# Performance work log

Hardware: AMD Instinct MI355X
Metric: run time of the kernel (lower is better)

Reference implementation:

```python
import jax, jax.numpy as jnp
import numpy as np

B, S, D, E, H, TOPK = 4, 1024, 512, 8, 1536, 2
NORM_EPS = 1e-5

def _ln(x, w, b, eps=1e-5):
    m = jnp.mean(x, -1, keepdims=True)
    v = jnp.var(x, -1, keepdims=True)  # biased var, as torch LayerNorm
    return (x - m) * jax.lax.rsqrt(v + eps) * w + b

def _modulate(x, shift, scale):
    return x * (1 + scale[:, None, :]) + shift[:, None, :]

def setup_inputs() -> dict:
    key = jax.random.key(0)
    ks = jax.random.split(key, 14)
    s = 0.02
    return dict(
        x=jax.random.normal(ks[0], (B, S, D), jnp.float32),
        c=jax.random.normal(ks[1], (B, D), jnp.float32),
        W_ada=jax.random.normal(ks[2], (D, 6 * D), jnp.float32) * s,
        b_ada=jax.random.normal(ks[3], (6 * D,), jnp.float32) * 0.1,
        Wq=jax.random.normal(ks[4], (D, D), jnp.float32) * s,
        Wk=jax.random.normal(ks[5], (D, D), jnp.float32) * s,
        Wv=jax.random.normal(ks[6], (D, D), jnp.float32) * s,
        Wo=jax.random.normal(ks[7], (D, D), jnp.float32) * s,
        qn_w=jnp.ones((D,), jnp.float32), qn_b=jnp.zeros((D,), jnp.float32),
        kn_w=jnp.ones((D,), jnp.float32), kn_b=jnp.zeros((D,), jnp.float32),
        an_w=jnp.ones((D,), jnp.float32), an_b=jnp.zeros((D,), jnp.float32),
        fn_w=jnp.ones((D,), jnp.float32), fn_b=jnp.zeros((D,), jnp.float32),
        Wr=jax.random.normal(ks[8], (D, E), jnp.float32) * s,
        br=jnp.zeros((E,), jnp.float32),
        W1=jax.random.normal(ks[9], (E, D, H), jnp.float32) * s,
        W2=jax.random.normal(ks[10], (E, H, D), jnp.float32) * s,
        W3=jax.random.normal(ks[11], (E, D, H), jnp.float32) * s,
    )

def reference(x, c, W_ada, b_ada, Wq, Wk, Wv, Wo, qn_w, qn_b, kn_w, kn_b,
              an_w, an_b, fn_w, fn_b, Wr, br, W1, W2, W3):
    # adaLN conditioning: SiLU -> Linear -> 6 chunks
    mods = jax.nn.silu(c) @ W_ada + b_ada          # (B, 6D)
    sh_msa, sc_msa, g_msa, sh_mlp, sc_mlp, g_mlp = jnp.split(mods, 6, axis=1)

    # Attention (source attends over the FEATURE dim: scores are (B, D, D))
    h = _modulate(_ln(x, an_w, an_b, NORM_EPS), sh_msa, sc_msa)
    q = _ln(h @ Wq, qn_w, qn_b)
    k = _ln(h @ Wk, kn_w, kn_b)
    v = h @ Wv
    scores = jnp.einsum('bsd,bse->bde', q, k)      # (B, D, D), no 1/sqrt scale (as source)
    A = jax.nn.softmax(scores, axis=-1)
    attn = jnp.einsum('bde,bse->bsd', A, v) @ Wo   # (B, S, D)
    x = x + g_msa[:, None, :] * attn

    # MoE feed-forward (top-2 routing; output REPLACES x, no residual/gate per source)
    xm = _modulate(_ln(x, fn_w, fn_b, NORM_EPS), sh_mlp, sc_mlp)
    logits = xm @ Wr + br                          # (B, S, E)
    # F.normalize default dim=1 -> L2 normalize over the SEQUENCE axis (faithful)
    nrm = jnp.sqrt(jnp.sum(logits * logits, axis=1, keepdims=True))
    logits = logits / jnp.maximum(nrm, 1e-12)
    probs = jax.nn.softmax(logits, axis=-1)        # (B, S, E)
    vals, idx = jax.lax.top_k(probs, TOPK)

    T = B * S
    xf = xm.reshape(T, D)
    # dense combine weights: zero for unselected experts (same math as gather/scatter-add)
    wden = jnp.zeros((T, E), xf.dtype).at[jnp.arange(T)[:, None], idx.reshape(T, TOPK)].set(vals.reshape(T, TOPK))
    h1 = jnp.einsum('td,edh->teh', xf, W1)
    h3 = jnp.einsum('td,edh->teh', xf, W3)
    y = jnp.einsum('teh,ehd->ted', jnp.sin(h1) * h3, W2)  # sin-gated FFN per expert
    moe = jnp.einsum('ted,te->td', y, wden).reshape(B, S, D)

    avg = probs.mean(axis=0)                       # mean over batch dim only (faithful): (S, E)
    aux = jnp.sum((1.0 / E - avg) ** 2)
    return moe, aux
```

## Files before the change

kernel.cpp:

```cpp
#include <hip/hip_runtime.h>
#include <math.h>

#define NB 4
#define NS 1024
#define ND 512
#define NE 8
#define NH 1536
#define NT 4096
#define D6 3072

typedef _Float16 half_t;
typedef _Float16 f16x8 __attribute__((ext_vector_type(8)));
typedef _Float16 f16x4 __attribute__((ext_vector_type(4)));
typedef float    f32x4 __attribute__((ext_vector_type(4)));

#define LDC 136
#define TM_MAX 71

__device__ __forceinline__ void gld16(const void* g, void* l) {
  __builtin_amdgcn_global_load_lds((const __attribute__((address_space(1))) char*)g,
                                   (__attribute__((address_space(3))) char*)l, 16, 0, 0);
}

__device__ __forceinline__ int resolve_tile(const int* __restrict__ offs, int t,
                                            int& e_out, int& m0_out) {
  int acc = 0, found = 0, ee = 0, mm = 0;
  #pragma unroll
  for (int q = 0; q < NE; ++q) {
    int ne_q = offs[q + 1] - offs[q];
    int te = (ne_q + 127) >> 7;
    if (!found && t < acc + te) { ee = q; mm = (t - acc) << 7; found = 1; }
    acc += te;
  }
  e_out = ee; m0_out = mm;
  return found;
}

__global__ __launch_bounds__(256) void k_ada(const float* __restrict__ c,
    const float* __restrict__ Wada, const float* __restrict__ bada,
    float* __restrict__ mods)
{
  __shared__ float sc[ND];
  __shared__ float part[256];
  int tid = threadIdx.x;
  int blk = blockIdx.x;
  int o0 = blk * 64;
  int b = o0 / D6;
  int j0 = o0 - b * D6;
  for (int d = tid; d < ND; d += 256) {
    float v = c[b * ND + d];
    sc[d] = v / (1.f + expf(-v));
  }
  __syncthreads();
  int j = j0 + (tid & 63);
  int kc = tid >> 6;
  float acc = 0.f;
  #pragma unroll 8
  for (int d = kc * 128; d < kc * 128 + 128; ++d)
    acc += sc[d] * Wada[(size_t)d * D6 + j];
  part[tid] = acc;
  __syncthreads();
  if (tid < 64) {
    float r = part[tid] + part[tid + 64] + part[tid + 128] + part[tid + 192]
            + bada[j0 + tid];
    mods[b * D6 + j0 + tid] = r;
  }
}

__global__ __launch_bounds__(256) void k_lnmod(const float* X, int xstride,
    float* Yf, half_t* Yh, half_t* Yl, int ystride,
    const float* __restrict__ w, const float* __restrict__ b,
    const float* __restrict__ mods, int sh_off, int sc_off,
    const float* __restrict__ Wr, const float* __restrict__ br,
    float* __restrict__ logits)
{
  __shared__ float red[16];
  __shared__ float red2[32];
  int tid = threadIdx.x;
  int row = blockIdx.x;
  int batch = row >> 10;
  const float* xr = X + (size_t)row * xstride;
  float x0 = xr[tid], x1 = xr[tid + 256];
  float s = x0 + x1, q = x0 * x0 + x1 * x1;
  #pragma unroll
  for (int off = 32; off > 0; off >>= 1) { s += __shfl_down(s, off, 64); q += __shfl_down(q, off, 64); }
  if ((tid & 63) == 0) { red[tid >> 6] = s; red[8 + (tid >> 6)] = q; }
  __syncthreads();
  if (tid == 0) {
    float S = red[0] + red[1] + red[2] + red[3];
    float Q = red[8] + red[9] + red[10] + red[11];
    float mean = S * (1.f / (float)ND);
    float var = Q * (1.f / (float)ND) - mean * mean;
    red[0] = mean; red[1] = rsqrtf(var + 1e-5f);
  }
  __syncthreads();
  float mean = red[0], rstd = red[1];
  int d0 = tid, d1 = tid + 256;
  float y0 = (x0 - mean) * rstd * w[d0] + b[d0];
  float y1 = (x1 - mean) * rstd * w[d1] + b[d1];
  if (mods) {
    const float* mb = mods + batch * D6;
    y0 = y0 * (1.f + mb[sc_off + d0]) + mb[sh_off + d0];
    y1 = y1 * (1.f + mb[sc_off + d1]) + mb[sh_off + d1];
  }
  size_t o0 = (size_t)row * ystride + d0, o1 = (size_t)row * ystride + d1;
  if (Yf) { Yf[o0] = y0; Yf[o1] = y1; }
  if (Yh) {
    half_t h0 = (half_t)y0, h1 = (half_t)y1;
    Yh[o0] = h0; Yh[o1] = h1;
    if (Yl) { Yl[o0] = (half_t)(y0 - (float)h0); Yl[o1] = (half_t)(y1 - (float)h1); }
  }
  if (Wr) {
    float p[8];
    float4 wa = *(const float4*)(Wr + d0 * 8);
    float4 wb = *(const float4*)(Wr + d0 * 8 + 4);
    float4 wc = *(const float4*)(Wr + d1 * 8);
    float4 wd = *(const float4*)(Wr + d1 * 8 + 4);
    p[0] = y0 * wa.x + y1 * wc.x; p[1] = y0 * wa.y + y1 * wc.y;
    p[2] = y0 * wa.z + y1 * wc.z; p[3] = y0 * wa.w + y1 * wc.w;
    p[4] = y0 * wb.x + y1 * wd.x; p[5] = y0 * wb.y + y1 * wd.y;
    p[6] = y0 * wb.z + y1 * wd.z; p[7] = y0 * wb.w + y1 * wd.w;
    #pragma unroll
    for (int off = 32; off > 0; off >>= 1)
      #pragma unroll
      for (int e = 0; e < 8; ++e) p[e] += __shfl_down(p[e], off, 64);
    if ((tid & 63) == 0) {
      #pragma unroll
      for (int e = 0; e < 8; ++e) red2[(tid >> 6) * 8 + e] = p[e];
    }
    __syncthreads();
    if (tid < 8)
      logits[(size_t)row * 8 + tid] = red2[tid] + red2[8 + tid] + red2[16 + tid]
                                    + red2[24 + tid] + br[tid];
  }
}

__global__ __launch_bounds__(256) void k_lnqk(float* QKV,
    const float* __restrict__ qw, const float* __restrict__ qb,
    const float* __restrict__ kw, const float* __restrict__ kb)
{
  __shared__ float red[16];
  int tid = threadIdx.x;
  int row = blockIdx.x >> 1;
  int h = blockIdx.x & 1;
  const float* w = h ? kw : qw;
  const float* b = h ? kb : qb;
  float* xr = QKV + (size_t)row * 1536 + h * 512;
  float x0 = xr[tid], x1 = xr[tid + 256];
  float s = x0 + x1, q = x0 * x0 + x1 * x1;
  #pragma unroll
  for (int off = 32; off > 0; off >>= 1) { s += __shfl_down(s, off, 64); q += __shfl_down(q, off, 64); }
  if ((tid & 63) == 0) { red[tid >> 6] = s; red[8 + (tid >> 6)] = q; }
  __syncthreads();
  if (tid == 0) {
    float S = red[0] + red[1] + red[2] + red[3];
    float Q = red[8] + red[9] + red[10] + red[11];
    float mean = S * (1.f / (float)ND);
    float var = Q * (1.f / (float)ND) - mean * mean;
    red[0] = mean; red[1] = rsqrtf(var + 1e-5f);
  }
  __syncthreads();
  float mean = red[0], rstd = red[1];
  xr[tid]       = (x0 - mean) * rstd * w[tid] + b[tid];
  xr[tid + 256] = (x1 - mean) * rstd * w[tid + 256] + b[tid + 256];
}

__global__ __launch_bounds__(256) void k_tsplit2(const float* __restrict__ QKV,
    half_t* __restrict__ H0, half_t* __restrict__ L0)
{
  __shared__ float tile[32][33];
  int z = blockIdx.z;
  half_t* outH = H0 + (size_t)z * 4194304;
  half_t* outL = L0 + (size_t)z * 4194304;
  int col0 = z * 512;
  int s0 = blockIdx.x * 32, c0 = blockIdx.y * 32;
  int tid = threadIdx.x;
  int r = tid >> 5, c = tid & 31;
  #pragma unroll
  for (int p = 0; p < 4; ++p)
    tile[r + p * 8][c] = QKV[(size_t)(s0 + r + p * 8) * 1536 + col0 + c0 + c];
  __syncthreads();
  #pragma unroll
  for (int p = 0; p < 4; ++p) {
    float v = tile[c][r + p * 8];
    half_t h = (half_t)v;
    size_t o = (size_t)(c0 + r + p * 8) * NT + s0 + c;
    outH[o] = h; outL[o] = (half_t)(v - (float)h);
  }
}

__global__ __launch_bounds__(256) void k_wsplit4(const float* __restrict__ Wq,
    const float* __restrict__ Wk, const float* __restrict__ Wv,
    const float* __restrict__ Wo, half_t* __restrict__ outH, half_t* __restrict__ outL)
{
  __shared__ float tile[32][33];
  int z = blockIdx.z;
  const float* W = (z == 0) ? Wq : (z == 1) ? Wk : (z == 2) ? Wv : Wo;
  int rowoff = z * 512;
  int k0 = blockIdx.x * 32, n0 = blockIdx.y * 32;
  int tid = threadIdx.x;
  int r = tid >> 5, c = tid & 31;
  #pragma unroll
  for (int p = 0; p < 4; ++p)
    tile[r + p * 8][c] = W[(size_t)(k0 + r + p * 8) * ND + n0 + c];
  __syncthreads();
  #pragma unroll
  for (int p = 0; p < 4; ++p) {
    float v = tile[c][r + p * 8];
    half_t h = (half_t)v;
    size_t o = (size_t)(rowoff + n0 + r + p * 8) * ND + k0 + c;
    outH[o] = h; outL[o] = (half_t)(v - (float)h);
  }
}

__global__ __launch_bounds__(256) void k_vsplit(const float* __restrict__ QKV,
    half_t* __restrict__ Vh, half_t* __restrict__ Vl)
{
  int i = blockIdx.x * 256 + threadIdx.x;
  int s = i >> 7, c = (i & 127) * 4;
  float4 v = *(const float4*)(QKV + (size_t)s * 1536 + 1024 + c);
  f16x4 h, l;
  h[0] = (half_t)v.x; l[0] = (half_t)(v.x - (float)h[0]);
  h[1] = (half_t)v.y; l[1] = (half_t)(v.y - (float)h[1]);
  h[2] = (half_t)v.z; l[2] = (half_t)(v.z - (float)h[2]);
  h[3] = (half_t)v.w; l[3] = (half_t)(v.w - (float)h[3]);
  *(f16x4*)(Vh + (size_t)s * ND + c) = h;
  *(f16x4*)(Vl + (size_t)s * ND + c) = l;
}

template<int MODE>
__global__ __launch_bounds__(256, 2) void k_gemm_hl(
    const half_t* __restrict__ Ah, const half_t* __restrict__ Al, long long sAz,
    const half_t* __restrict__ Bh, const half_t* __restrict__ Bl, long long sBz,
    int lda, int ldb, int K,
    float* __restrict__ Cf, half_t* __restrict__ Ch, half_t* __restrict__ Cl,
    long long sCz, int ldc,
    const float* __restrict__ xres, const float* __restrict__ mods)
{
  int z = blockIdx.z;
  int m0 = blockIdx.x * 128, n0 = blockIdx.y * 128;
  __shared__ __align__(16) char smem[65536];
  half_t* Sh = (half_t*)smem;
  int tid = threadIdx.x;
  int lane = tid & 63, w = tid >> 6;
  int wm = (w >> 1) * 64, wn = (w & 1) * 64;
  int qd = lane >> 4, md = lane & 15;
  int rA0 = tid >> 2;
  int sw = (((tid & 3) ^ ((tid >> 3) & 3)) << 3);

  const half_t* pAh0 = Ah + z * sAz + (size_t)(m0 + rA0) * lda + sw;
  const half_t* pAh1 = pAh0 + (size_t)64 * lda;
  const half_t* pAl0 = Al + z * sAz + (size_t)(m0 + rA0) * lda + sw;
  const half_t* pAl1 = pAl0 + (size_t)64 * lda;
  const half_t* pBh0 = Bh + z * sBz + (size_t)(n0 + rA0) * ldb + sw;
  const half_t* pBh1 = pBh0 + (size_t)64 * ldb;
  const half_t* pBl0 = Bl + z * sBz + (size_t)(n0 + rA0) * ldb + sw;
  const half_t* pBl1 = pBl0 + (size_t)64 * ldb;

  char* dAh = smem + w * 1024;
  char* dAl = smem + 16384 + w * 1024;
  char* dBh = smem + 32768 + w * 1024;
  char* dBl = smem + 49152 + w * 1024;

  f32x4 acc[4][4];
  #pragma unroll
  for (int i = 0; i < 4; ++i)
    #pragma unroll
    for (int j = 0; j < 4; ++j)
      #pragma unroll
      for (int p = 0; p < 4; ++p) acc[i][j][p] = 0.f;

  int swq  = ((qd ^ ((md >> 1) & 3)) << 3);
  int aoff = (wm + md) * 32 + swq;
  int boff = (wn + md) * 32 + swq;

#define GEMM_STAGE(p, kk) do { int kb_ = (kk); int pb_ = (p) * 8192;         \
    gld16(pAh0 + kb_, dAh + pb_); gld16(pAh1 + kb_, dAh + pb_ + 4096);       \
    gld16(pAl0 + kb_, dAl + pb_); gld16(pAl1 + kb_, dAl + pb_ + 4096);       \
    gld16(pBh0 + kb_, dBh + pb_); gld16(pBh1 + kb_, dBh + pb_ + 4096);       \
    gld16(pBl0 + kb_, dBl + pb_); gld16(pBl1 + kb_, dBl + pb_ + 4096); } while (0)

  int iters = K >> 5;
  GEMM_STAGE(0, 0);
  int cur = 0;
  #pragma unroll 1
  for (int it = 0; it < iters; ++it) {
    if (it + 1 < iters) {
      GEMM_STAGE(cur ^ 1, (it + 1) * 32);
      asm volatile("s_waitcnt vmcnt(8)\ns_barrier" ::: "memory");
    } else {
      asm volatile("s_waitcnt vmcnt(0)\ns_barrier" ::: "memory");
    }
    const half_t* Ash = Sh + cur * 4096;
    const half_t* Asl = Sh + 8192  + cur * 4096;
    const half_t* Bsh = Sh + 16384 + cur * 4096;
    const half_t* Bsl = Sh + 24576 + cur * 4096;
    f16x8 ah[4], al[4], bh[4], bl[4];
    #pragma unroll
    for (int i = 0; i < 4; ++i) {
      ah[i] = *(const f16x8*)(Ash + aoff + i * 512);
      al[i] = *(const f16x8*)(Asl + aoff + i * 512);
    }
    #pragma unroll
    for (int j = 0; j < 4; ++j) {
      bh[j] = *(const f16x8*)(Bsh + boff + j * 512);
      bl[j] = *(const f16x8*)(Bsl + boff + j * 512);
    }
    __builtin_amdgcn_s_setprio(1);
    #pragma unroll
    for (int i = 0; i < 4; ++i)
      #pragma unroll
      for (int j = 0; j < 4; ++j) {
        acc[i][j] = __builtin_amdgcn_mfma_f32_16x16x32_f16(ah[i], bh[j], acc[i][j], 0, 0, 0);
        acc[i][j] = __builtin_amdgcn_mfma_f32_16x16x32_f16(ah[i], bl[j], acc[i][j], 0, 0, 0);
        acc[i][j] = __builtin_amdgcn_mfma_f32_16x16x32_f16(al[i], bh[j], acc[i][j], 0, 0, 0);
      }
    __builtin_amdgcn_s_setprio(0);
    asm volatile("s_barrier" ::: "memory");
    cur ^= 1;
  }
#undef GEMM_STAGE

  if (MODE == 1) {
    half_t* Cs = (half_t*)smem;
    __syncthreads();
    #pragma unroll
    for (int i = 0; i < 4; ++i)
      #pragma unroll
      for (int j = 0; j < 4; ++j)
        #pragma unroll
        for (int p = 0; p < 4; ++p)
          Cs[(wm + 16 * i + qd * 4 + p) * LDC + wn + 16 * j + md] = (half_t)acc[i][j][p];
    __syncthreads();
    #pragma unroll
    for (int it2 = 0; it2 < 8; ++it2) {
      int chunk = it2 * 256 + tid;
      int r = chunk >> 4, c8 = (chunk & 15) * 8;
      *(f16x8*)(Ch + z * sCz + (size_t)(m0 + r) * ldc + n0 + c8) = *(const f16x8*)(Cs + r * LDC + c8);
    }
    __syncthreads();
    #pragma unroll
    for (int i = 0; i < 4; ++i)
      #pragma unroll
      for (int j = 0; j < 4; ++j)
        #pragma unroll
        for (int p = 0; p < 4; ++p) {
          float v = acc[i][j][p];
          half_t h = (half_t)v;
          Cs[(wm + 16 * i + qd * 4 + p) * LDC + wn + 16 * j + md] = (half_t)(v - (float)h);
        }
    __syncthreads();
    #pragma unroll
    for (int it2 = 0; it2 < 8; ++it2) {
      int chunk = it2 * 256 + tid;
      int r = chunk >> 4, c8 = (chunk & 15) * 8;
      *(f16x8*)(Cl + z * sCz + (size_t)(m0 + r) * ldc + n0 + c8) = *(const f16x8*)(Cs + r * LDC + c8);
    }
  } else {
    #pragma unroll
    for (int i = 0; i < 4; ++i)
      #pragma unroll
      for (int p = 0; p < 4; ++p) {
        int r = m0 + wm + 16 * i + qd * 4 + p;
        float* cp = Cf + z * sCz + (size_t)r * ldc + n0 + wn + md;
        if (MODE == 2) {
          int batch = r >> 10;
          const float* mb = mods + batch * D6 + 2 * ND;
          const float* xp = xres + (size_t)r * ldc + n0 + wn + md;
          #pragma unroll
          for (int j = 0; j < 4; ++j) {
            int col = wn + md + 16 * j;
            cp[16 * j] = xp[16 * j] + mb[n0 + col] * acc[i][j][p];
          }
        } else {
          #pragma unroll
          for (int j = 0; j < 4; ++j) cp[16 * j] = acc[i][j][p];
        }
      }
  }
}

__global__ __launch_bounds__(256) void k_softmax512_sum4(const float* __restrict__ SC4,
    half_t* __restrict__ Ph, half_t* __restrict__ Pl)
{
  __shared__ float red[16];
  int tid = threadIdx.x;
  int row = blockIdx.x;
  int b = row >> 9, d = row & 511;
  const float* r0 = SC4 + ((size_t)(b * 4 + 0) << 18) + (size_t)d * ND;
  const float* r1 = SC4 + ((size_t)(b * 4 + 1) << 18) + (size_t)d * ND;
  const float* r2 = SC4 + ((size_t)(b * 4 + 2) << 18) + (size_t)d * ND;
  const float* r3 = SC4 + ((size_t)(b * 4 + 3) << 18) + (size_t)d * ND;
  float x0 = r0[tid] + r1[tid] + r2[tid] + r3[tid];
  float x1 = r0[tid + 256] + r1[tid + 256] + r2[tid + 256] + r3[tid + 256];
  float m = fmaxf(x0, x1);
  #pragma unroll
  for (int off = 32; off > 0; off >>= 1) m = fmaxf(m, __shfl_down(m, off, 64));
  if ((tid & 63) == 0) red[tid >> 6] = m;
  __syncthreads();
  if (tid == 0) red[0] = fmaxf(fmaxf(red[0], red[1]), fmaxf(red[2], red[3]));
  __syncthreads();
  m = red[0];
  float e0 = expf(x0 - m), e1 = expf(x1 - m);
  float s = e0 + e1;
  #pragma unroll
  for (int off = 32; off > 0; off >>= 1) s += __shfl_down(s, off, 64);
  if ((tid & 63) == 0) red[8 + (tid >> 6)] = s;
  __syncthreads();
  if (tid == 0) red[8] = red[8] + red[9] + red[10] + red[11];
  __syncthreads();
  float inv = 1.f / red[8];
  float p0 = e0 * inv, p1 = e1 * inv;
  size_t base = (size_t)row * ND;
  half_t h0 = (half_t)p0, h1 = (half_t)p1;
  Ph[base + tid] = h0;       Pl[base + tid] = (half_t)(p0 - (float)h0);
  Ph[base + tid + 256] = h1; Pl[base + tid + 256] = (half_t)(p1 - (float)h1);
}

__global__ __launch_bounds__(256) void k_colnorm(const float* __restrict__ logits,
    float* __restrict__ nrm)
{
  __shared__ float red[8];
  int tid = threadIdx.x;
  int b = blockIdx.x >> 3, e = blockIdx.x & 7;
  float acc = 0.f;
  for (int s = tid; s < NS; s += 256) {
    float l = logits[((size_t)(b << 10) + s) * NE + e];
    acc += l * l;
  }
  #pragma unroll
  for (int off = 32; off > 0; off >>= 1) acc += __shfl_down(acc, off, 64);
  if ((tid & 63) == 0) red[tid >> 6] = acc;
  __syncthreads();
  if (tid == 0) nrm[b * NE + e] = sqrtf(red[0] + red[1] + red[2] + red[3]);
}

__global__ __launch_bounds__(1024) void k_route(const float* __restrict__ logits,
    const float* __restrict__ nrm, float* __restrict__ probs,
    float* __restrict__ wsel, int* __restrict__ offs_g,
    int* __restrict__ list, int* __restrict__ inv)
{
  __shared__ unsigned char sisel[8192];
  __shared__ int cw[8][16][8];
  __shared__ int soffs[9];
  __shared__ float snrm[32];
  int tid = threadIdx.x;
  int lane = tid & 63, wv = tid >> 6;
  if (tid < 32) snrm[tid] = fmaxf(nrm[tid], 1e-12f);
  __syncthreads();
  #pragma unroll 1
  for (int c = 0; c < 4; ++c) {
    int t = c * 1024 + tid;
    int b = t >> 10;
    float p[8];
    float4 l0 = *(const float4*)(logits + (size_t)t * 8);
    float4 l1 = *(const float4*)(logits + (size_t)t * 8 + 4);
    p[0] = l0.x / snrm[b * 8 + 0]; p[1] = l0.y / snrm[b * 8 + 1];
    p[2] = l0.z / snrm[b * 8 + 2]; p[3] = l0.w / snrm[b * 8 + 3];
    p[4] = l1.x / snrm[b * 8 + 4]; p[5] = l1.y / snrm[b * 8 + 5];
    p[6] = l1.z / snrm[b * 8 + 6]; p[7] = l1.w / snrm[b * 8 + 7];
    float mx = p[0];
    #pragma unroll
    for (int e = 1; e < 8; ++e) mx = fmaxf(mx, p[e]);
    float s = 0.f;
    #pragma unroll
    for (int e = 0; e < 8; ++e) { p[e] = expf(p[e] - mx); s += p[e]; }
    float invs = 1.f / s;
    #pragma unroll
    for (int e = 0; e < 8; ++e) { p[e] *= invs; probs[(size_t)t * 8 + e] = p[e]; }
    int i1 = 0;
    #pragma unroll
    for (int e = 1; e < 8; ++e) if (p[e] > p[i1]) i1 = e;
    int i2 = (i1 == 0) ? 1 : 0;
    #pragma unroll
    for (int e = 0; e < 8; ++e) if (e != i1 && p[e] > p[i2]) i2 = e;
    wsel[t * 2] = p[i1]; wsel[t * 2 + 1] = p[i2];
    sisel[t * 2] = (unsigned char)i1; sisel[t * 2 + 1] = (unsigned char)i2;
  }
  __syncthreads();
  #pragma unroll 1
  for (int c = 0; c < 8; ++c) {
    int em = sisel[c * 1024 + tid];
    #pragma unroll
    for (int e = 0; e < 8; ++e) {
      unsigned long long mask = __ballot(em == e);
      if (lane == 0) cw[c][wv][e] = (int)__popcll(mask);
    }
  }
  __syncthreads();
  if (tid < 8) {
    int e = tid, run = 0;
    for (int c = 0; c < 8; ++c)
      for (int w2 = 0; w2 < 16; ++w2) { int v = cw[c][w2][e]; cw[c][w2][e] = run; run += v; }
    soffs[e] = run;
  }
  __syncthreads();
  if (tid == 0) {
    int a = 0;
    #pragma unroll
    for (int e = 0; e < 8; ++e) { int v = soffs[e]; soffs[e] = a; a += v; }
    soffs[8] = a;
  }
  __syncthreads();
  if (tid < 9) offs_g[tid] = soffs[tid];
  #pragma unroll 1
  for (int c = 0; c < 8; ++c) {
    int idx = c * 1024 + tid;
    int em = sisel[idx];
    int rk = 0;
    #pragma unroll
    for (int e = 0; e < 8; ++e) {
      unsigned long long mask = __ballot(em == e);
      if (em == e) rk = (int)__popcll(mask & ((1ull << lane) - 1ull));
    }
    int slot = soffs[em] + cw[c][wv][em] + rk;
    list[slot] = idx >> 1;
    inv[idx] = slot;
  }
}

__global__ __launch_bounds__(256) void k_aux(const float* __restrict__ probs,
    float* __restrict__ outAux)
{
  __shared__ float red[8];
  int tid = threadIdx.x;
  float acc = 0.f;
  for (int s = tid; s < NS; s += 256) {
    #pragma unroll
    for (int e = 0; e < NE; ++e) {
      float a = probs[(size_t)s * NE + e] + probs[(size_t)(NS + s) * NE + e]
              + probs[(size_t)(2 * NS + s) * NE + e] + probs[(size_t)(3 * NS + s) * NE + e];
      float d = 0.125f - a * 0.25f;
      acc += d * d;
    }
  }
  #pragma unroll
  for (int off = 32; off > 0; off >>= 1) acc += __shfl_down(acc, off, 64);
  if ((tid & 63) == 0) red[tid >> 6] = acc;
  __syncthreads();
  if (tid == 0) *outAux = red[0] + red[1] + red[2] + red[3];
}

__global__ __launch_bounds__(256) void k_tcast13(const float* __restrict__ W1,
    const float* __restrict__ W3, half_t* __restrict__ W1t, half_t* __restrict__ W3t)
{
  __shared__ float tile[32][33];
  int z = blockIdx.z;
  int sel = z >> 3, e = z & 7;
  const float* We = (sel ? W3 : W1) + (size_t)e * ND * NH;
  half_t* Wte = (sel ? W3t : W1t) + (size_t)e * ND * NH;
  int k0 = blockIdx.x * 32, n0 = blockIdx.y * 32;
  int tid = threadIdx.x;
  int r = tid >> 5, c = tid & 31;
  #pragma unroll
  for (int p = 0; p < 4; ++p)
    tile[r + p * 8][c] = We[(size_t)(k0 + r + p * 8) * NH + n0 + c];
  __syncthreads();
  #pragma unroll
  for (int p = 0; p < 4; ++p)
    Wte[(size_t)(n0 + r + p * 8) * ND + k0 + c] = (half_t)tile[c][r + p * 8];
}

__global__ __launch_bounds__(256) void k_tcastW2(const float* __restrict__ W,
    half_t* __restrict__ Wt)
{
  __shared__ float tile[32][33];
  const float* We = W + (size_t)blockIdx.z * NH * ND;
  half_t* Wte = Wt + (size_t)blockIdx.z * NH * ND;
  int k0 = blockIdx.x * 32, n0 = blockIdx.y * 32;
  int tid = threadIdx.x;
  int r = tid >> 5, c = tid & 31;
  #pragma unroll
  for (int p = 0; p < 4; ++p)
    tile[r + p * 8][c] = We[(size_t)(k0 + r + p * 8) * ND + n0 + c];
  __syncthreads();
  #pragma unroll
  for (int p = 0; p < 4; ++p)
    Wte[(size_t)(n0 + r + p * 8) * NH + k0 + c] = (half_t)tile[c][r + p * 8];
}

__global__ __launch_bounds__(256, 3) void k_ffn_fused(const half_t* __restrict__ xmh,
    const half_t* __restrict__ W1t, const half_t* __restrict__ W3t,
    const int* __restrict__ list, const int* __restrict__ offs,
    half_t* __restrict__ gate)
{
  int bx = blockIdx.x;
  int n0 = (bx % 12) * 128;
  int t  = bx / 12;
  int e, m0;
  if (!resolve_tile(offs, t, e, m0)) return;
  int base = offs[e], ne = offs[e + 1] - base;

  __shared__ __align__(16) char smem[49664];
  half_t* Sh = (half_t*)smem;
  int* rowt = (int*)(smem + 49152);
  int tid = threadIdx.x;
  if (tid < 128) {
    int rr = m0 + tid;
    rowt[tid] = (rr < ne) ? list[base + rr] : 0;
  }
  __syncthreads();

  int lane = tid & 63, w = tid >> 6;
  int wm = (w >> 1) * 64, wn = (w & 1) * 64;
  int qd = lane >> 4, md = lane & 15;
  int rA0 = tid >> 2;
  int sw = (((tid & 3) ^ ((tid >> 3) & 3)) << 3);
  int tok0 = rowt[rA0], tok1 = rowt[rA0 + 64];

  const half_t* gA0  = xmh + (size_t)tok0 * ND + sw;
  const half_t* gA1  = xmh + (size_t)tok1 * ND + sw;
  const half_t* gB10 = W1t + ((size_t)e * NH + n0 + rA0) * ND + sw;
  const half_t* gB11 = gB10 + (size_t)64 * ND;
  const half_t* gB30 = W3t + ((size_t)e * NH + n0 + rA0) * ND + sw;
  const half_t* gB31 = gB30 + (size_t)64 * ND;

  char* dA  = smem + w * 1024;
  char* dB1 = smem + 16384 + w * 1024;
  char* dB3 = smem + 32768 + w * 1024;

  f32x4 acc1[4][4], acc3[4][4];
  #pragma unroll
  for (int i = 0; i < 4; ++i)
    #pragma unroll
    for (int j = 0; j < 4; ++j)
      #pragma unroll
      for (int p = 0; p < 4; ++p) { acc1[i][j][p] = 0.f; acc3[i][j][p] = 0.f; }

  int swq  = ((qd ^ ((md >> 1) & 3)) << 3);
  int aoff = (wm + md) * 32 + swq;
  int boff = (wn + md) * 32 + swq;

#define FFN_STAGE(p, kk) do { int kb_ = (kk); int pb_ = (p) * 8192;          \
    gld16(gA0  + kb_, dA  + pb_); gld16(gA1  + kb_, dA  + pb_ + 4096);       \
    gld16(gB10 + kb_, dB1 + pb_); gld16(gB11 + kb_, dB1 + pb_ + 4096);       \
    gld16(gB30 + kb_, dB3 + pb_); gld16(gB31 + kb_, dB3 + pb_ + 4096); } while (0)

  FFN_STAGE(0, 0);
  int cur = 0;
  #pragma unroll 1
  for (int it = 0; it < 16; ++it) {
    if (it + 1 < 16) {
      FFN_STAGE(cur ^ 1, (it + 1) * 32);
      asm volatile("s_waitcnt vmcnt(6)\ns_barrier" ::: "memory");
    } else {
      asm volatile("s_waitcnt vmcnt(0)\ns_barrier" ::: "memory");
    }
    const half_t* As  = Sh + cur * 4096;
    const half_t* B1s = Sh + 8192  + cur * 4096;
    const half_t* B3s = Sh + 16384 + cur * 4096;
    f16x8 a[4];
    #pragma unroll
    for (int i = 0; i < 4; ++i) a[i] = *(const f16x8*)(As + aoff + i * 512);
    __builtin_amdgcn_s_setprio(1);
    #pragma unroll
    for (int j = 0; j < 4; ++j) {
      f16x8 b1 = *(const f16x8*)(B1s + boff + j * 512);
      f16x8 b3 = *(const f16x8*)(B3s + boff + j * 512);
      #pragma unroll
      for (int i = 0; i < 4; ++i) {
        acc1[i][j] = __builtin_amdgcn_mfma_f32_16x16x32_f16(a[i], b1, acc1[i][j], 0, 0, 0);
        acc3[i][j] = __builtin_amdgcn_mfma_f32_16x16x32_f16(a[i], b3, acc3[i][j], 0, 0, 0);
      }
    }
    __builtin_amdgcn_s_setprio(0);
    asm volatile("s_barrier" ::: "memory");
    cur ^= 1;
  }
#undef FFN_STAGE

  half_t* Cs = (half_t*)smem;
  #pragma unroll
  for (int i = 0; i < 4; ++i)
    #pragma unroll
    for (int j = 0; j < 4; ++j)
      #pragma unroll
      for (int p = 0; p < 4; ++p) {
        int rr = wm + 16 * i + qd * 4 + p;
        int cc = wn + 16 * j + md;
        Cs[rr * LDC + cc] = (half_t)(__sinf(acc1[i][j][p]) * acc3[i][j][p]);
      }
  __syncthreads();
  #pragma unroll
  for (int it = 0; it < 8; ++it) {
    int chunk = it * 256 + tid;
    int rr = chunk >> 4, c8 = (chunk & 15) * 8;
    if (m0 + rr < ne) {
      *(f16x8*)(gate + (size_t)(base + m0 + rr) * NH + n0 + c8) = *(const f16x8*)(Cs + rr * LDC + c8);
    }
  }
}

__global__ __launch_bounds__(256, 4) void k_moe2_mfma(const half_t* __restrict__ gate,
    const half_t* __restrict__ W2t, const int* __restrict__ offs,
    float* __restrict__ P)
{
  int bx = blockIdx.x;
  int n0 = (bx & 3) * 128;
  int t = bx >> 2;
  int e, m0;
  if (!resolve_tile(offs, t, e, m0)) return;
  int base = offs[e], ne = offs[e + 1] - base;

  __shared__ __align__(16) char smem[32768];
  half_t* Sh = (half_t*)smem;
  int tid = threadIdx.x;
  int lane = tid & 63, w = tid >> 6;
  int wm = (w >> 1) * 64, wn = (w & 1) * 64;
  int qd = lane >> 4, md = lane & 15;
  int rA0 = tid >> 2;
  int sw = (((tid & 3) ^ ((tid >> 3) & 3)) << 3);

  int ar0 = m0 + rA0;      if (ar0 >= ne) ar0 = ne - 1;
  int ar1 = m0 + rA0 + 64; if (ar1 >= ne) ar1 = ne - 1;
  const half_t* gA0 = gate + (size_t)(base + ar0) * NH + sw;
  const half_t* gA1 = gate + (size_t)(base + ar1) * NH + sw;
  const half_t* gB0 = W2t + ((size_t)e * ND + n0 + rA0) * NH + sw;
  const half_t* gB1 = gB0 + (size_t)64 * NH;

  char* dA = smem + w * 1024;
  char* dB = smem + 16384 + w * 1024;

  f32x4 acc[4][4];
  #pragma unroll
  for (int i = 0; i < 4; ++i)
    #pragma unroll
    for (int j = 0; j < 4; ++j)
      #pragma unroll
      for (int p = 0; p < 4; ++p) acc[i][j][p] = 0.f;

  int swq  = ((qd ^ ((md >> 1) & 3)) << 3);
  int aoff = (wm + md) * 32 + swq;
  int boff = (wn + md) * 32 + swq;

#define MOE2_STAGE(p, kk) do { int kb_ = (kk); int pb_ = (p) * 8192;         \
    gld16(gA0 + kb_, dA + pb_); gld16(gA1 + kb_, dA + pb_ + 4096);           \
    gld16(gB0 + kb_, dB + pb_); gld16(gB1 + kb_, dB + pb_ + 4096); } while (0)

  MOE2_STAGE(0, 0);
  int cur = 0;
  #pragma unroll 1
  for (int it = 0; it < 48; ++it) {
    if (it + 1 < 48) {
      MOE2_STAGE(cur ^ 1, (it + 1) * 32);
      asm volatile("s_waitcnt vmcnt(4)\ns_barrier" ::: "memory");
    } else {
      asm volatile("s_waitcnt vmcnt(0)\ns_barrier" ::: "memory");
    }
    const half_t* As = Sh + cur * 4096;
    const half_t* Bs = Sh + 8192 + cur * 4096;
    f16x8 a[4];
    #pragma unroll
    for (int i = 0; i < 4; ++i) a[i] = *(const f16x8*)(As + aoff + i * 512);
    __builtin_amdgcn_s_setprio(1);
    #pragma unroll
    for (int j = 0; j < 4; ++j) {
      f16x8 b = *(const f16x8*)(Bs + boff + j * 512);
      #pragma unroll
      for (int i = 0; i < 4; ++i)
        acc[i][j] = __builtin_amdgcn_mfma_f32_16x16x32_f16(a[i], b, acc[i][j], 0, 0, 0);
    }
    __builtin_amdgcn_s_setprio(0);
    asm volatile("s_barrier" ::: "memory");
    cur ^= 1;
  }
#undef MOE2_STAGE

  #pragma unroll
  for (int i = 0; i < 4; ++i)
    #pragma unroll
    for (int p = 0; p < 4; ++p) {
      int gr = m0 + wm + 16 * i + qd * 4 + p;
      if (gr < ne) {
        float* pp = P + (size_t)(base + gr) * ND + n0 + wn + md;
        #pragma unroll
        for (int j = 0; j < 4; ++j)
          pp[16 * j] = acc[i][j][p];
      }
    }
}

__global__ __launch_bounds__(256) void k_moe_reduce(const float* __restrict__ P,
    const int* __restrict__ inv, const float* __restrict__ wsel,
    float* __restrict__ out)
{
  int i = blockIdx.x * 256 + threadIdx.x;
  int t = i >> 7, d4 = i & 127;
  int s1 = inv[t * 2], s2 = inv[t * 2 + 1];
  float w1 = wsel[t * 2], w2 = wsel[t * 2 + 1];
  const float4* P4 = (const float4*)P;
  float4 a = P4[(size_t)s1 * 128 + d4];
  float4 b = P4[(size_t)s2 * 128 + d4];
  float4 o;
  o.x = w1 * a.x + w2 * b.x;
  o.y = w1 * a.y + w2 * b.y;
  o.z = w1 * a.z + w2 * b.z;
  o.w = w1 * a.w + w2 * b.w;
  ((float4*)out)[i] = o;
}

static const size_t BO_MODS  = 0;
static const size_t BO_HH    = 65536;
static const size_t BO_HL2   = 4259840;
static const size_t BO_PH    = 4259840;
static const size_t BO_PL    = 6357056;
static const size_t BO_WALLH = 8454144;
static const size_t BO_WALLL = 10551296;
static const size_t BO_QKV   = 12648448;
static const size_t BO_A0H   = 12648448;
static const size_t BO_A0L   = 16842752;
static const size_t BO_SC4   = 21037056;
static const size_t BO_X2    = 21037056;
static const size_t BO_XM    = 29425664;
static const size_t BO_QTH   = 37814272;
static const size_t BO_QTL   = 42008576;
static const size_t BO_KTH   = 46202880;
static const size_t BO_KTL   = 50397184;
static const size_t BO_VH    = 54591488;
static const size_t BO_VL    = 58785792;
static const size_t BO_W1T   = 37814272;
static const size_t BO_XMH   = 50397184;
static const size_t BO_W3T   = 65536;
static const size_t BO_GATE  = 12648448;
static const size_t BO_W2T   = 65536;
static const size_t BO_P     = 37814272;
static const size_t BO_LOGI  = 62980096;
static const size_t BO_NRM   = 63111168;
static const size_t BO_PROB  = 63111296;
static const size_t BO_WSEL  = 63242368;
static const size_t BO_INTS  = 63307904;

extern "C" void kernel_launch(void* const* d_in, const int* in_sizes, int n_in,
                              void* d_out, int out_size, void* d_ws, size_t ws_size,
                              hipStream_t stream)
{
  const float* x    = (const float*)d_in[0];
  const float* c    = (const float*)d_in[1];
  const float* Wada = (const float*)d_in[2];
  const float* bada = (const float*)d_in[3];
  const float* Wq   = (const float*)d_in[4];
  const float* Wk   = (const float*)d_in[5];
  const float* Wv   = (const float*)d_in[6];
  const float* Wo   = (const float*)d_in[7];
  const float* qn_w = (const float*)d_in[8];
  const float* qn_b = (const float*)d_in[9];
  const float* kn_w = (const float*)d_in[10];
  const float* kn_b = (const float*)d_in[11];
  const float* an_w = (const float*)d_in[12];
  const float* an_b = (const float*)d_in[13];
  const float* fn_w = (const float*)d_in[14];
  const float* fn_b = (const float*)d_in[15];
  const float* Wr   = (const float*)d_in[16];
  const float* br   = (const float*)d_in[17];
  const float* W1   = (const float*)d_in[18];
  const float* W2   = (const float*)d_in[19];
  const float* W3   = (const float*)d_in[20];
  float* out = (float*)d_out;
  char*  ws8 = (char*)d_ws;
  float* MODS = (float*)(ws8 + BO_MODS);
  half_t* Hh = (half_t*)(ws8 + BO_HH),   *Hl = (half_t*)(ws8 + BO_HL2);
  half_t* Ph = (half_t*)(ws8 + BO_PH),   *Pl = (half_t*)(ws8 + BO_PL);
  half_t* WALLH = (half_t*)(ws8 + BO_WALLH), *WALLL = (half_t*)(ws8 + BO_WALLL);
  half_t* WoTh = WALLH + (size_t)1536 * ND,  *WoTl = WALLL + (size_t)1536 * ND;
  float* QKV = (float*)(ws8 + BO_QKV);
  half_t* A0h = (half_t*)(ws8 + BO_A0H), *A0l = (half_t*)(ws8 + BO_A0L);
  float* SC4 = (float*)(ws8 + BO_SC4);
  float* X2  = (float*)(ws8 + BO_X2);
  float* XM  = (float*)(ws8 + BO_XM);
  half_t* qTh = (half_t*)(ws8 + BO_QTH), *qTl = (half_t*)(ws8 + BO_QTL);
  half_t* kTh = (half_t*)(ws8 + BO_KTH), *kTl = (half_t*)(ws8 + BO_KTL);
  half_t* Vh  = (half_t*)(ws8 + BO_VH),  *Vl  = (half_t*)(ws8 + BO_VL);
  half_t* W1T = (half_t*)(ws8 + BO_W1T);
  half_t* W3T = (half_t*)(ws8 + BO_W3T);
  half_t* W2T = (half_t*)(ws8 + BO_W2T);
  half_t* XMH = (half_t*)(ws8 + BO_XMH);
  half_t* GATEH = (half_t*)(ws8 + BO_GATE);
  float* PBUF = (float*)(ws8 + BO_P);
  float* LOGI = (float*)(ws8 + BO_LOGI);
  float* NRM  = (float*)(ws8 + BO_NRM);
  float* PROB = (float*)(ws8 + BO_PROB);
  float* WSEL = (float*)(ws8 + BO_WSEL);
  int* ib   = (int*)(ws8 + BO_INTS);
  int* offs = ib + 8208;
  int* list = ib + 8224;
  int* inv  = ib + 16416;

  k_ada<<<192, 256, 0, stream>>>(c, Wada, bada, MODS);
  k_wsplit4<<<dim3(16, 16, 4), 256, 0, stream>>>(Wq, Wk, Wv, Wo, WALLH, WALLL);
  k_lnmod<<<NT, 256, 0, stream>>>(x, ND, nullptr, Hh, Hl, ND, an_w, an_b, MODS, 0, 512,
                                  nullptr, nullptr, nullptr);
  k_gemm_hl<0><<<dim3(32, 12, 1), 256, 0, stream>>>(Hh, Hl, 0, WALLH, WALLL, 0,
      ND, ND, ND, QKV, nullptr, nullptr, 0, 1536, nullptr, nullptr);
  k_lnqk<<<2 * NT, 256, 0, stream>>>(QKV, qn_w, qn_b, kn_w, kn_b);
  k_tsplit2<<<dim3(128, 16, 2), 256, 0, stream>>>(QKV, qTh, qTl);
  k_vsplit<<<2048, 256, 0, stream>>>(QKV, Vh, Vl);
  k_gemm_hl<0><<<dim3(4, 4, 16), 256, 0, stream>>>(qTh, qTl, 256, kTh, kTl, 256,
      NT, NT, 256, SC4, nullptr, nullptr, 262144, ND, nullptr, nullptr);
  k_softmax512_sum4<<<2048, 256, 0, stream>>>(SC4, Ph, Pl);
  k_gemm_hl<1><<<dim3(8, 4, 4), 256, 0, stream>>>(Vh, Vl, 524288, Ph, Pl, 262144,
      ND, ND, ND, nullptr, A0h, A0l, 524288, ND, nullptr, nullptr);
  k_gemm_hl<2><<<dim3(32, 4, 1), 256, 0, stream>>>(A0h, A0l, 0, WoTh, WoTl, 0,
      ND, ND, ND, X2, nullptr, nullptr, 0, ND, x, MODS);
  k_lnmod<<<NT, 256, 0, stream>>>(X2, ND, XM, XMH, nullptr, ND, fn_w, fn_b, MODS, 1536, 2048,
                                  Wr, br, LOGI);
  k_colnorm<<<32, 256, 0, stream>>>(LOGI, NRM);
  k_route<<<1, 1024, 0, stream>>>(LOGI, NRM, PROB, WSEL, offs, list, inv);
  k_aux<<<1, 256, 0, stream>>>(PROB, out + (size_t)NT * ND);
  k_tcast13<<<dim3(16, 48, 16), 256, 0, stream>>>(W1, W3, W1T, W3T);
  k_ffn_fused<<<TM_MAX * 12, 256, 0, stream>>>(XMH, W1T, W3T, list, offs, GATEH);
  k_tcastW2<<<dim3(48, 16, 8), 256, 0, stream>>>(W2, W2T);
  k_moe2_mfma<<<TM_MAX * 4, 256, 0, stream>>>(GATEH, W2T, offs, PBUF);
  k_moe_reduce<<<2048, 256, 0, stream>>>(PBUF, inv, WSEL, out);
}
```

Baseline: 394.8 us.

## Halve MoE GEMM N-tiles and load FFN A operand directly into registers

The fused W1/W3 FFN kernel and the W2 expert GEMM drop from 128-wide to 64-wide N tiles, which doubles the grid and cuts LDS use and accumulator registers, so more blocks can be resident per CU. In the FFN kernel the gathered token rows (A operand) are no longer staged through LDS. Each lane loads its MFMA fragment straight from global memory into registers, double-buffered across an unrolled two-stage loop. The cost is that A and B data are each fetched twice as often overall, and the direct gathered loads may be less coalesced.

Measured after the change: 431.7 us. 9.4% more time.

```diff
diff --git a/kernel.cpp b/kernel.cpp
--- a/kernel.cpp
+++ b/kernel.cpp
@@ -15,6 +15,7 @@
 typedef float    f32x4 __attribute__((ext_vector_type(4)));
 
 #define LDC 136
+#define LDC2 72
 #define TM_MAX 71
 
 __device__ __forceinline__ void gld16(const void* g, void* l) {
@@ -585,15 +586,15 @@
     half_t* __restrict__ gate)
 {
   int bx = blockIdx.x;
-  int n0 = (bx % 12) * 128;
-  int t  = bx / 12;
+  int n0 = (bx % 24) * 64;
+  int t  = bx / 24;
   int e, m0;
   if (!resolve_tile(offs, t, e, m0)) return;
   int base = offs[e], ne = offs[e + 1] - base;
 
-  __shared__ __align__(16) char smem[49664];
+  __shared__ __align__(16) char smem[18944];
   half_t* Sh = (half_t*)smem;
-  int* rowt = (int*)(smem + 49152);
+  int* rowt = (int*)(smem + 18432);
   int tid = threadIdx.x;
   if (tid < 128) {
     int rr = m0 + tid;
@@ -602,91 +603,103 @@
   __syncthreads();
 
   int lane = tid & 63, w = tid >> 6;
-  int wm = (w >> 1) * 64, wn = (w & 1) * 64;
+  int wm = (w >> 1) * 64, wn = (w & 1) * 32;
   int qd = lane >> 4, md = lane & 15;
-  int rA0 = tid >> 2;
-  int sw = (((tid & 3) ^ ((tid >> 3) & 3)) << 3);
-  int tok0 = rowt[rA0], tok1 = rowt[rA0 + 64];
-
-  const half_t* gA0  = xmh + (size_t)tok0 * ND + sw;
-  const half_t* gA1  = xmh + (size_t)tok1 * ND + sw;
-  const half_t* gB10 = W1t + ((size_t)e * NH + n0 + rA0) * ND + sw;
-  const half_t* gB11 = gB10 + (size_t)64 * ND;
-  const half_t* gB30 = W3t + ((size_t)e * NH + n0 + rA0) * ND + sw;
-  const half_t* gB31 = gB30 + (size_t)64 * ND;
-
-  char* dA  = smem + w * 1024;
-  char* dB1 = smem + 16384 + w * 1024;
-  char* dB3 = smem + 32768 + w * 1024;
-
-  f32x4 acc1[4][4], acc3[4][4];
+  int rB = tid >> 2;
+  int swB = (((tid & 3) ^ ((rB >> 1) & 3)) << 3);
+
+  const half_t* gB1 = W1t + ((size_t)e * NH + n0 + rB) * ND + swB;
+  const half_t* gB3 = W3t + ((size_t)e * NH + n0 + rB) * ND + swB;
+  char* dB1 = smem + w * 1024;
+  char* dB3 = smem + 8192 + w * 1024;
+
+  const half_t* pa0 = xmh + (size_t)rowt[wm + md] * ND + qd * 8;
+  const half_t* pa1 = xmh + (size_t)rowt[wm + 16 + md] * ND + qd * 8;
+  const half_t* pa2 = xmh + (size_t)rowt[wm + 32 + md] * ND + qd * 8;
+  const half_t* pa3 = xmh + (size_t)rowt[wm + 48 + md] * ND + qd * 8;
+
+  f32x4 acc1[4][2], acc3[4][2];
   #pragma unroll
   for (int i = 0; i < 4; ++i)
     #pragma unroll
-    for (int j = 0; j < 4; ++j)
+    for (int j = 0; j < 2; ++j)
       #pragma unroll
       for (int p = 0; p < 4; ++p) { acc1[i][j][p] = 0.f; acc3[i][j][p] = 0.f; }
 
   int swq  = ((qd ^ ((md >> 1) & 3)) << 3);
-  int aoff = (wm + md) * 32 + swq;
   int boff = (wn + md) * 32 + swq;
 
-#define FFN_STAGE(p, kk) do { int kb_ = (kk); int pb_ = (p) * 8192;          \
-    gld16(gA0  + kb_, dA  + pb_); gld16(gA1  + kb_, dA  + pb_ + 4096);       \
-    gld16(gB10 + kb_, dB1 + pb_); gld16(gB11 + kb_, dB1 + pb_ + 4096);       \
-    gld16(gB30 + kb_, dB3 + pb_); gld16(gB31 + kb_, dB3 + pb_ + 4096); } while (0)
-
-  FFN_STAGE(0, 0);
-  int cur = 0;
+#define FFN_STAGE_B(p, kk) do { int kb_ = (kk);                              \
+    gld16(gB1 + kb_, dB1 + (p) * 4096); gld16(gB3 + kb_, dB3 + (p) * 4096); } while (0)
+#define FFN_LOAD_A(ar, kk) do { int ka_ = (kk);                              \
+    ar[0] = *(const f16x8*)(pa0 + ka_); ar[1] = *(const f16x8*)(pa1 + ka_);  \
+    ar[2] = *(const f16x8*)(pa2 + ka_); ar[3] = *(const f16x8*)(pa3 + ka_); } while (0)
+#define FFN_COMPUTE(cur, ar) do {                                            \
+    const half_t* B1s = Sh + (cur) * 2048;                                   \
+    const half_t* B3s = Sh + 4096 + (cur) * 2048;                            \
+    f16x8 b1[2], b3[2];                                                      \
+    _Pragma("unroll")                                                        \
+    for (int j = 0; j < 2; ++j) {                                            \
+      b1[j] = *(const f16x8*)(B1s + boff + j * 512);                         \
+      b3[j] = *(const f16x8*)(B3s + boff + j * 512);                         \
+    }                                                                        \
+    __builtin_amdgcn_s_setprio(1);                                           \
+    _Pragma("unroll")                                                        \
+    for (int j = 0; j < 2; ++j)                                              \
+      _Pragma("unroll")                                                      \
+      for (int i = 0; i < 4; ++i) {                                          \
+        acc1[i][j] = __builtin_amdgcn_mfma_f32_16x16x32_f16(ar[i], b1[j], acc1[i][j], 0, 0, 0); \
+        acc3[i][j] = __builtin_amdgcn_mfma_f32_16x16x32_f16(ar[i], b3[j], acc3[i][j], 0, 0, 0); \
+      }                                                                      \
+    __builtin_amdgcn_s_setprio(0);                                           \
+  } while (0)
+
+  f16x8 a0_[4], a1_[4];
+  FFN_STAGE_B(0, 0);
+  FFN_LOAD_A(a0_, 0);
   #pragma unroll 1
-  for (int it = 0; it < 16; ++it) {
+  for (int it = 0; it < 16; it += 2) {
     if (it + 1 < 16) {
-      FFN_STAGE(cur ^ 1, (it + 1) * 32);
+      FFN_STAGE_B(1, (it + 1) * 32);
+      FFN_LOAD_A(a1_, (it + 1) * 32);
       asm volatile("s_waitcnt vmcnt(6)\ns_barrier" ::: "memory");
     } else {
       asm volatile("s_waitcnt vmcnt(0)\ns_barrier" ::: "memory");
     }
-    const half_t* As  = Sh + cur * 4096;
-    const half_t* B1s = Sh + 8192  + cur * 4096;
-    const half_t* B3s = Sh + 16384 + cur * 4096;
-    f16x8 a[4];
-    #pragma unroll
-    for (int i = 0; i < 4; ++i) a[i] = *(const f16x8*)(As + aoff + i * 512);
-    __builtin_amdgcn_s_setprio(1);
-    #pragma unroll
-    for (int j = 0; j < 4; ++j) {
-      f16x8 b1 = *(const f16x8*)(B1s + boff + j * 512);
-      f16x8 b3 = *(const f16x8*)(B3s + boff + j * 512);
-      #pragma unroll
-      for (int i = 0; i < 4; ++i) {
-        acc1[i][j] = __builtin_amdgcn_mfma_f32_16x16x32_f16(a[i], b1, acc1[i][j], 0, 0, 0);
-        acc3[i][j] = __builtin_amdgcn_mfma_f32_16x16x32_f16(a[i], b3, acc3[i][j], 0, 0, 0);
-      }
-    }
-    __builtin_amdgcn_s_setprio(0);
+    FFN_COMPUTE(0, a0_);
     asm volatile("s_barrier" ::: "memory");
-    cur ^= 1;
-  }
-#undef FFN_STAGE
+    if (it + 2 < 16) {
+      FFN_STAGE_B(0, (it + 2) * 32);
+      FFN_LOAD_A(a0_, (it + 2) * 32);
+      asm volatile("s_waitcnt vmcnt(6)\ns_barrier" ::: "memory");
+    } else {
+      asm volatile("s_waitcnt vmcnt(0)\ns_barrier" ::: "memory");
+    }
+    FFN_COMPUTE(1, a1_);
+    asm volatile("s_barrier" ::: "memory");
+  }
+#undef FFN_STAGE_B
+#undef FFN_LOAD_A
+#undef FFN_COMPUTE
 
   half_t* Cs = (half_t*)smem;
   #pragma unroll
   for (int i = 0; i < 4; ++i)
     #pragma unroll
-    for (int j = 0; j < 4; ++j)
+    for (int j = 0; j < 2; ++j)
       #pragma unroll
       for (int p = 0; p < 4; ++p) {
         int rr = wm + 16 * i + qd * 4 + p;
         int cc = wn + 16 * j + md;
-        Cs[rr * LDC + cc] = (half_t)(__sinf(acc1[i][j][p]) * acc3[i][j][p]);
+        Cs[rr * LDC2 + cc] = (half_t)(__sinf(acc1[i][j][p]) * acc3[i][j][p]);
       }
   __syncthreads();
   #pragma unroll
-  for (int it = 0; it < 8; ++it) {
+  for (int it = 0; it < 4; ++it) {
     int chunk = it * 256 + tid;
-    int rr = chunk >> 4, c8 = (chunk & 15) * 8;
+    int rr = chunk >> 3, c8 = (chunk & 7) * 8;
     if (m0 + rr < ne) {
-      *(f16x8*)(gate + (size_t)(base + m0 + rr) * NH + n0 + c8) = *(const f16x8*)(Cs + rr * LDC + c8);
+      *(f16x8*)(gate + (size_t)(base + m0 + rr) * NH + n0 + c8) = *(const f16x8*)(Cs + rr * LDC2 + c8);
     }
   }
 }
@@ -696,17 +709,17 @@
     float* __restrict__ P)
 {
   int bx = blockIdx.x;
-  int n0 = (bx & 3) * 128;
-  int t = bx >> 2;
+  int n0 = (bx & 7) * 64;
+  int t = bx >> 3;
   int e, m0;
   if (!resolve_tile(offs, t, e, m0)) return;
   int base = offs[e], ne = offs[e + 1] - base;
 
-  __shared__ __align__(16) char smem[32768];
+  __shared__ __align__(16) char smem[24576];
   half_t* Sh = (half_t*)smem;
   int tid = threadIdx.x;
   int lane = tid & 63, w = tid >> 6;
-  int wm = (w >> 1) * 64, wn = (w & 1) * 64;
+  int wm = (w >> 1) * 64, wn = (w & 1) * 32;
   int qd = lane >> 4, md = lane & 15;
   int rA0 = tid >> 2;
   int sw = (((tid & 3) ^ ((tid >> 3) & 3)) << 3);
@@ -716,16 +729,15 @@
   const half_t* gA0 = gate + (size_t)(base + ar0) * NH + sw;
   const half_t* gA1 = gate + (size_t)(base + ar1) * NH + sw;
   const half_t* gB0 = W2t + ((size_t)e * ND + n0 + rA0) * NH + sw;
-  const half_t* gB1 = gB0 + (size_t)64 * NH;
 
   char* dA = smem + w * 1024;
   char* dB = smem + 16384 + w * 1024;
 
-  f32x4 acc[4][4];
+  f32x4 acc[4][2];
   #pragma unroll
   for (int i = 0; i < 4; ++i)
     #pragma unroll
-    for (int j = 0; j < 4; ++j)
+    for (int j = 0; j < 2; ++j)
       #pragma unroll
       for (int p = 0; p < 4; ++p) acc[i][j][p] = 0.f;
 
@@ -733,9 +745,9 @@
   int aoff = (wm + md) * 32 + swq;
   int boff = (wn + md) * 32 + swq;
 
-#define MOE2_STAGE(p, kk) do { int kb_ = (kk); int pb_ = (p) * 8192;         \
-    gld16(gA0 + kb_, dA + pb_); gld16(gA1 + kb_, dA + pb_ + 4096);           \
-    gld16(gB0 + kb_, dB + pb_); gld16(gB1 + kb_, dB + pb_ + 4096); } while (0)
+#define MOE2_STAGE(p, kk) do { int kb_ = (kk);                               \
+    gld16(gA0 + kb_, dA + (p) * 8192); gld16(gA1 + kb_, dA + (p) * 8192 + 4096); \
+    gld16(gB0 + kb_, dB + (p) * 4096); } while (0)
 
   MOE2_STAGE(0, 0);
   int cur = 0;
@@ -743,23 +755,23 @@
   for (int it = 0; it < 48; ++it) {
     if (it + 1 < 48) {
       MOE2_STAGE(cur ^ 1, (it + 1) * 32);
-      asm volatile("s_waitcnt vmcnt(4)\ns_barrier" ::: "memory");
+      asm volatile("s_waitcnt vmcnt(3)\ns_barrier" ::: "memory");
     } else {
       asm volatile("s_waitcnt vmcnt(0)\ns_barrier" ::: "memory");
     }
     const half_t* As = Sh + cur * 4096;
-    const half_t* Bs = Sh + 8192 + cur * 4096;
-    f16x8 a[4];
+    const half_t* Bs = Sh + 8192 + cur * 2048;
+    f16x8 a[4], b[2];
     #pragma unroll
     for (int i = 0; i < 4; ++i) a[i] = *(const f16x8*)(As + aoff + i * 512);
+    #pragma unroll
+    for (int j = 0; j < 2; ++j) b[j] = *(const f16x8*)(Bs + boff + j * 512);
     __builtin_amdgcn_s_setprio(1);
     #pragma unroll
-    for (int j = 0; j < 4; ++j) {
-      f16x8 b = *(const f16x8*)(Bs + boff + j * 512);
+    for (int j = 0; j < 2; ++j)
       #pragma unroll
       for (int i = 0; i < 4; ++i)
-        acc[i][j] = __builtin_amdgcn_mfma_f32_16x16x32_f16(a[i], b, acc[i][j], 0, 0, 0);
-    }
+        acc[i][j] = __builtin_amdgcn_mfma_f32_16x16x32_f16(a[i], b[j], acc[i][j], 0, 0, 0);
     __builtin_amdgcn_s_setprio(0);
     asm volatile("s_barrier" ::: "memory");
     cur ^= 1;
@@ -774,7 +786,7 @@
       if (gr < ne) {
         float* pp = P + (size_t)(base + gr) * ND + n0 + wn + md;
         #pragma unroll
-        for (int j = 0; j < 4; ++j)
+        for (int j = 0; j < 2; ++j)
           pp[16 * j] = acc[i][j][p];
       }
     }
@@ -907,8 +919,8 @@
   k_route<<<1, 1024, 0, stream>>>(LOGI, NRM, PROB, WSEL, offs, list, inv);
   k_aux<<<1, 256, 0, stream>>>(PROB, out + (size_t)NT * ND);
   k_tcast13<<<dim3(16, 48, 16), 256, 0, stream>>>(W1, W3, W1T, W3T);
-  k_ffn_fused<<<TM_MAX * 12, 256, 0, stream>>>(XMH, W1T, W3T, list, offs, GATEH);
+  k_ffn_fused<<<TM_MAX * 24, 256, 0, stream>>>(XMH, W1T, W3T, list, offs, GATEH);
   k_tcastW2<<<dim3(48, 16, 8), 256, 0, stream>>>(W2, W2T);
-  k_moe2_mfma<<<TM_MAX * 4, 256, 0, stream>>>(GATEH, W2T, offs, PBUF);
+  k_moe2_mfma<<<TM_MAX * 8, 256, 0, stream>>>(GATEH, W2T, offs, PBUF);
   k_moe_reduce<<<2048, 256, 0, stream>>>(PBUF, inv, WSEL, out);
 }
```
